# Kernel optimization log

Measured on AMD Instinct MI355X. Metric: run time of the kernel, lower is better.

## Reference

```python
import jax, jax.numpy as jnp
import numpy as np
import math

B, NI, NU, D, H, MAXNB, T = 1024, 50000, 20000, 256, 4, 20, 1000


def _cosine_sqrt_ab():
    t = jnp.linspace(0.0, T, T + 1) / T
    ab = jnp.cos((t + 0.008) / 1.008 * math.pi / 2) ** 2
    ab = ab / ab[0]
    ab = ab[1:]
    return jnp.sqrt(ab), jnp.sqrt(1.0 - ab)


def _ln(x, g, b, eps=1e-5):
    m = jnp.mean(x, -1, keepdims=True)
    v = jnp.var(x, -1, keepdims=True)
    return (x - m) / jnp.sqrt(v + eps) * g + b


def _mha(q, k, v, wqkv, bqkv, wo, bo):
    # torch nn.MultiheadAttention (batch_first) with packed in_proj
    d = q.shape[-1]
    dh = d // H
    wq, wk, wv = jnp.split(wqkv, 3, axis=0)
    bq, bk, bv = jnp.split(bqkv, 3, axis=0)
    def heads(x, w, bb):
        y = x @ w.T + bb
        return y.reshape(x.shape[0], x.shape[1], H, dh).transpose(0, 2, 1, 3)
    qh, kh, vh = heads(q, wq, bq), heads(k, wk, bk), heads(v, wv, bv)
    att = jax.nn.softmax(jnp.einsum('bhqd,bhkd->bhqk', qh, kh) / math.sqrt(dh), axis=-1)
    o = jnp.einsum('bhqk,bhkd->bhqd', att, vh)
    o = o.transpose(0, 2, 1, 3).reshape(q.shape[0], q.shape[1], d)
    return o @ wo.T + bo


def setup_inputs() -> dict:
    key = jax.random.key(0)
    ks = iter(jax.random.split(key, 64))
    p = lambda shape, s=0.02: jax.random.normal(next(ks), shape, jnp.float32) * s
    inp = {}
    inp['x0'] = (jax.random.uniform(next(ks), (B, NI)) < 0.05).astype(jnp.float32)
    inp['user_ids'] = jax.random.randint(next(ks), (B,), 0, NU)
    inp['t'] = jax.random.randint(next(ks), (B,), 0, T)
    inp['noise'] = jax.random.normal(next(ks), (B, D), jnp.float32)
    inp['neighbor_idx'] = jax.random.randint(next(ks), (NU, MAXNB), 0, NI)
    inp['item_emb'] = p((NI, D), 0.01)
    inp['enc_w1'] = p((2 * D, NI), 0.01); inp['enc_b1'] = jnp.zeros((2 * D,))
    inp['enc_w2'] = p((D, 2 * D)); inp['enc_b2'] = jnp.zeros((D,))
    inp['dec_w1'] = p((2 * D, D)); inp['dec_b1'] = jnp.zeros((2 * D,))
    inp['dec_w2'] = p((NI, 2 * D)); inp['dec_b2'] = jnp.zeros((NI,))
    inp['up_w'] = p((D, D)); inp['up_b'] = jnp.zeros((D,))
    inp['ip_w'] = p((D, D)); inp['ip_b'] = jnp.zeros((D,))
    inp['te_w1'] = p((32, 1)); inp['te_b1'] = jnp.zeros((32,))
    inp['te_w2'] = p((D, 32)); inp['te_b2'] = jnp.zeros((D,))
    inp['ca_wqkv'] = p((3 * D, D)); inp['ca_bqkv'] = jnp.zeros((3 * D,))
    inp['ca_wo'] = p((D, D)); inp['ca_bo'] = jnp.zeros((D,))
    inp['sa_wqkv'] = p((3 * D, D)); inp['sa_bqkv'] = jnp.zeros((3 * D,))
    inp['sa_wo'] = p((D, D)); inp['sa_bo'] = jnp.zeros((D,))
    inp['n1_g'] = jnp.ones((D,)); inp['n1_b'] = jnp.zeros((D,))
    inp['n2_g'] = jnp.ones((D,)); inp['n2_b'] = jnp.zeros((D,))
    inp['ff_w1'] = p((2 * D, D)); inp['ff_b1'] = jnp.zeros((2 * D,))
    inp['ff_w2'] = p((D, 2 * D)); inp['ff_b2'] = jnp.zeros((D,))
    return inp


def reference(x0, user_ids, t, noise, neighbor_idx, item_emb,
              enc_w1, enc_b1, enc_w2, enc_b2, dec_w1, dec_b1, dec_w2, dec_b2,
              up_w, up_b, ip_w, ip_b, te_w1, te_b1, te_w2, te_b2,
              ca_wqkv, ca_bqkv, ca_wo, ca_bo, sa_wqkv, sa_bqkv, sa_wo, sa_bo,
              n1_g, n1_b, n2_g, n2_b, ff_w1, ff_b1, ff_w2, ff_b2):
    gelu = lambda x: jax.nn.gelu(x, approximate=False)
    # encoder: (B, NI) -> (B, D)
    z0 = gelu(x0 @ enc_w1.T + enc_b1) @ enc_w2.T + enc_b2
    sqrt_ab, sqrt_1ab = _cosine_sqrt_ab()
    z_t = sqrt_ab[t][:, None] * z0 + sqrt_1ab[t][:, None] * noise
    # vectorized padded neighbor gather: (B, MAXNB, D)
    nb = item_emb[neighbor_idx[user_ids]]
    t_norm = t.astype(jnp.float32) / T
    # denoiser
    q = (z_t @ up_w.T + up_b)[:, None, :]
    kv = nb @ ip_w.T + ip_b
    te = jax.nn.silu(t_norm[:, None] @ te_w1.T + te_b1) @ te_w2.T + te_b2
    q = q + te[:, None, :]
    ca = _mha(q, kv, kv, ca_wqkv, ca_bqkv, ca_wo, ca_bo)
    h = _ln(q + ca, n1_g, n1_b)[:, 0, :]
    sa = _mha(h[:, None], h[:, None], h[:, None], sa_wqkv, sa_bqkv, sa_wo, sa_bo)[:, 0, :]
    h = _ln(h + sa, n2_g, n2_b)
    z_pred = h + (gelu(h @ ff_w1.T + ff_b1) @ ff_w2.T + ff_b2)
    diff_loss = jnp.mean((z_pred - z0) ** 2)
    logits = gelu(z0 @ dec_w1.T + dec_b1) @ dec_w2.T + dec_b2
    recon = jnp.mean(jax.nn.softplus(logits) - logits * x0)
    return diff_loss + 0.1 * recon
```

## Files before the change

### kernel.cpp

```cpp
#include <hip/hip_runtime.h>
#include <math.h>

#define NI   50000
#define Tt   1000
#define KP   50176
#define MW   1568
#define NPAD 50048

typedef __bf16 bf16x8 __attribute__((ext_vector_type(8)));
typedef float  f32x4  __attribute__((ext_vector_type(4)));

__device__ __forceinline__ unsigned short f2bf(float f) {
  unsigned u = __float_as_uint(f);
  u += 0x7FFFu + ((u >> 16) & 1u);
  return (unsigned short)(u >> 16);
}
__device__ __forceinline__ float bf2f(unsigned short u) {
  return __uint_as_float(((unsigned)u) << 16);
}
__device__ __forceinline__ unsigned pack2(float a, float b) {
  return (unsigned)f2bf(a) | ((unsigned)f2bf(b) << 16);
}
__device__ __forceinline__ f32x4 mfma16(const unsigned short* a, const unsigned short* b, f32x4 c) {
  typedef unsigned short u16x8 __attribute__((ext_vector_type(8)));
  u16x8 av = *(const u16x8*)a;
  u16x8 bv = *(const u16x8*)b;
  return __builtin_amdgcn_mfma_f32_16x16x32_bf16(
      __builtin_bit_cast(bf16x8, av), __builtin_bit_cast(bf16x8, bv), c, 0, 0, 0);
}
__device__ __forceinline__ float gelu_f(float x) {
  return 0.5f * x * (1.f + erff(x * 0.70710678118654752f));
}

#define GLD16(gsrc, ldst) __builtin_amdgcn_global_load_lds( \
    (const __attribute__((address_space(1))) unsigned int*)(const void*)(gsrc), \
    (__attribute__((address_space(3))) unsigned int*)(void*)(ldst), 16, 0, 0)
#define GLD4(gsrc, ldst) __builtin_amdgcn_global_load_lds( \
    (const __attribute__((address_space(1))) unsigned int*)(const void*)(gsrc), \
    (__attribute__((address_space(3))) unsigned int*)(void*)(ldst), 4, 0, 0)

#define PIPE_FENCE() __builtin_amdgcn_sched_barrier(0)
#define RAW_BAR()    __builtin_amdgcn_s_barrier()

__global__ __launch_bounds__(256) void prep_crit(
    const float* __restrict__ x0, unsigned int* __restrict__ xmask,
    unsigned int* __restrict__ xmaskT,
    const float* __restrict__ enc_w1, unsigned short* __restrict__ w1b)
{
  __shared__ unsigned int T[32][64];
  __shared__ unsigned int nib[256];
  const int id = blockIdx.x, tid = threadIdx.x;
  if (id < 800) {
    int rg = id / 25, ch = id % 25;
    int r0 = rg * 32, c0 = ch * 2048, c0w = ch * 64;
    for (int rr = 0; rr < 32; ++rr) {
      int k = c0 + tid * 8;
      const float* row = x0 + (size_t)(r0 + rr) * NI;
      float4 a = make_float4(0.f, 0.f, 0.f, 0.f), b = a;
      if (k + 8 <= NI) {
        a = *(const float4*)(row + k);
        b = *(const float4*)(row + k + 4);
      }
      unsigned bits8 =
          (a.x != 0.f ? 1u : 0u)  | (a.y != 0.f ? 2u : 0u)  |
          (a.z != 0.f ? 4u : 0u)  | (a.w != 0.f ? 8u : 0u)  |
          (b.x != 0.f ? 16u : 0u) | (b.y != 0.f ? 32u : 0u) |
          (b.z != 0.f ? 64u : 0u) | (b.w != 0.f ? 128u : 0u);
      nib[tid] = bits8;
      __syncthreads();
      if (tid < 64) {
        T[rr][tid] = nib[tid * 4] | (nib[tid * 4 + 1] << 8) |
                     (nib[tid * 4 + 2] << 16) | (nib[tid * 4 + 3] << 24);
      }
      __syncthreads();
    }
    {
      int rr = tid >> 3, wg = (tid & 7) * 8;
      if (c0w + wg < MW) {
        unsigned* dst = xmask + (size_t)(r0 + rr) * MW + c0w + wg;
        uint4 q0 = make_uint4(T[rr][wg], T[rr][wg+1], T[rr][wg+2], T[rr][wg+3]);
        uint4 q1 = make_uint4(T[rr][wg+4], T[rr][wg+5], T[rr][wg+6], T[rr][wg+7]);
        *(uint4*)dst = q0; *(uint4*)(dst + 4) = q1;
      }
    }
    {
      int ww = tid >> 2, rg8 = (tid & 3) * 8;
      if (c0w + ww < MW) {
        unsigned* dst = xmaskT + (size_t)(c0w + ww) * 1024 + r0 + rg8;
        uint4 q0 = make_uint4(T[rg8][ww], T[rg8+1][ww], T[rg8+2][ww], T[rg8+3][ww]);
        uint4 q1 = make_uint4(T[rg8+4][ww], T[rg8+5][ww], T[rg8+6][ww], T[rg8+7][ww]);
        *(uint4*)dst = q0; *(uint4*)(dst + 4) = q1;
      }
    }
  } else {
    int r = id - 800;
    const float* s = enc_w1 + (size_t)r * NI;
    for (int ch = 0; ch < 25; ++ch) {
      int c = ch * 2048 + tid * 8;
      if (c >= KP) continue;
      uint4 o;
      if (c + 8 <= NI) {
        float4 a = *(const float4*)(s + c), b = *(const float4*)(s + c + 4);
        o.x = pack2(a.x, a.y); o.y = pack2(a.z, a.w);
        o.z = pack2(b.x, b.y); o.w = pack2(b.z, b.w);
      } else {
        float v[8];
#pragma unroll
        for (int i = 0; i < 8; ++i) v[i] = (c + i < NI) ? s[c + i] : 0.f;
        o.x = pack2(v[0], v[1]); o.y = pack2(v[2], v[3]);
        o.z = pack2(v[4], v[5]); o.w = pack2(v[6], v[7]);
      }
      *(uint4*)(w1b + (size_t)r * KP + c) = o;
    }
  }
}

#define EF_ENC  1024
#define EF_W2N  2592
#define EF_MANY 3040
#define EF_COMP 3808
#define EF_TE   4832

__global__ __launch_bounds__(256) void enc_fused(
    const unsigned int* __restrict__ xmaskT,
    const unsigned short* __restrict__ Bw,
    float* __restrict__ P0, float* __restrict__ P1,
    const float* __restrict__ dec_w2, unsigned short* __restrict__ w2n,
    const float* s0a, const float* s1a, const float* s2a, const float* s3a,
    const float* s4a, const float* s5a, const float* s6a,
    unsigned short* d0a, unsigned short* d1a, unsigned short* d2a, unsigned short* d3a,
    unsigned short* d4a, unsigned short* d5a, unsigned short* d6a,
    const float* __restrict__ ca_wqkv, const float* __restrict__ ca_bqkv,
    const float* __restrict__ ip_w, const float* __restrict__ ip_b,
    const float* __restrict__ sa_wqkv, const float* __restrict__ sa_bqkv,
    const float* __restrict__ sa_wo, const float* __restrict__ sa_bo,
    unsigned short* __restrict__ Wkv, float* __restrict__ bkv,
    unsigned short* __restrict__ Wsa, float* __restrict__ bsa,
    const int* __restrict__ t,
    const float* __restrict__ te_w1, const float* __restrict__ te_b1,
    const float* __restrict__ te_w2, const float* __restrict__ te_b2,
    float* __restrict__ te, float* __restrict__ sab, float* __restrict__ s1ab)
{
  __shared__ __align__(16) unsigned short BsE[2][2][128 * 32];
  __shared__ __align__(16) unsigned short lut[256][8];
  __shared__ unsigned int mskb[2][2][128];
  __shared__ float sj[32];
  const int id = blockIdx.x, tid = threadIdx.x;

  if (id < EF_ENC) {
    const int g = (id & 7) + 8 * (id >> 6);
    const int m0 = ((id >> 3) & 7) * 128;
    const int n0 = (g & 3) * 128;
    const int kc = g >> 2;
    const int kb = kc * 1568;
    const int kw0 = kc * 49;
    const int w = tid >> 6, l = tid & 63;
    const int wm = (w >> 1) * 64, wn = (w & 1) * 64;
    const int fr = l & 15, fo = (l >> 4) * 8;
    const int s0 = tid, s1 = tid + 256;
    const unsigned short* Br0 = Bw + (size_t)(n0 + (s0 >> 2)) * KP + kb + (s0 & 3) * 8;
    const unsigned short* Br1 = Bw + (size_t)(n0 + (s1 >> 2)) * KP + kb + (s1 & 3) * 8;
    f32x4 acc[4][4] = {};

    {
      unsigned b = (unsigned)tid;
      uint4 q;
      q.x = (b & 1u   ? 0x3F80u : 0u) | (b & 2u   ? 0x3F800000u : 0u);
      q.y = (b & 4u   ? 0x3F80u : 0u) | (b & 8u   ? 0x3F800000u : 0u);
      q.z = (b & 16u  ? 0x3F80u : 0u) | (b & 32u  ? 0x3F800000u : 0u);
      q.w = (b & 64u  ? 0x3F80u : 0u) | (b & 128u ? 0x3F800000u : 0u);
      *(uint4*)&lut[tid][0] = q;
    }

#define STGF(IT, BUF) do {                                                  \
    GLD4(xmaskT + (size_t)(kw0 + (IT) * 2 + (w & 1)) * 1024                 \
                + m0 + (w >> 1) * 64 + l,                                   \
         &mskb[BUF][w & 1][(w >> 1) * 64]);                                 \
    GLD16(Br0 + (IT) * 64,      &BsE[BUF][0][s0 * 8]);                      \
    GLD16(Br1 + (IT) * 64,      &BsE[BUF][0][s1 * 8]);                      \
    GLD16(Br0 + (IT) * 64 + 32, &BsE[BUF][1][s0 * 8]);                      \
    GLD16(Br1 + (IT) * 64 + 32, &BsE[BUF][1][s1 * 8]); } while (0)

#define STGT(BUF) do {                                                      \
    GLD4(xmaskT + (size_t)(kw0 + 48) * 1024 + m0 + (w & 1) * 64 + l,        \
         &mskb[BUF][0][(w & 1) * 64]);                                      \
    GLD16(Br0 + 24 * 64, &BsE[BUF][0][s0 * 8]);                             \
    GLD16(Br1 + 24 * 64, &BsE[BUF][0][s1 * 8]); } while (0)

#define CMPH(BUF, KK) do {                                                  \
    const unsigned short *ap_[4], *bp_[4];                                  \
    _Pragma("unroll") for (int i_ = 0; i_ < 4; ++i_)                        \
      ap_[i_] = &lut[(mskb[BUF][KK][wm + 16 * i_ + fr] >> fo) & 0xFF][0];   \
    _Pragma("unroll") for (int j_ = 0; j_ < 4; ++j_)                        \
      bp_[j_] = &BsE[BUF][KK][(wn + 16 * j_ + fr) * 32 + fo];               \
    _Pragma("unroll") for (int i_ = 0; i_ < 4; ++i_)                        \
    _Pragma("unroll") for (int j_ = 0; j_ < 4; ++j_)                        \
      acc[i_][j_] = mfma16(ap_[i_], bp_[j_], acc[i_][j_]); } while (0)

    STGF(0, 0);
    STGF(1, 1);
    asm volatile("s_waitcnt vmcnt(5) lgkmcnt(0)" ::: "memory");
    PIPE_FENCE(); RAW_BAR(); PIPE_FENCE();
    for (int it = 0; it < 24; ++it) {
      CMPH(it & 1, 0);
      CMPH(it & 1, 1);
      PIPE_FENCE(); RAW_BAR(); PIPE_FENCE();
      if (it < 22) {
        STGF(it + 2, it & 1);
        asm volatile("s_waitcnt vmcnt(5)" ::: "memory");
      } else if (it == 22) {
        STGT(0);
        asm volatile("s_waitcnt vmcnt(3)" ::: "memory");
      } else {
        asm volatile("s_waitcnt vmcnt(0)" ::: "memory");
      }
      PIPE_FENCE(); RAW_BAR(); PIPE_FENCE();
    }
    CMPH(0, 0);
#undef STGF
#undef STGT
#undef CMPH

    const int cr = (l >> 4) * 4, cc = l & 15;
    float* Cp = ((kc < 16) ? P0 : P1) + (size_t)(kc & 15) * 524288;
#pragma unroll
    for (int i = 0; i < 4; ++i)
#pragma unroll
      for (int j = 0; j < 4; ++j) {
        int n = n0 + wn + 16 * j + cc;
#pragma unroll
        for (int r = 0; r < 4; ++r) {
          int m = m0 + wm + 16 * i + cr + r;
          Cp[(size_t)m * 512 + n] = acc[i][j][r];
        }
      }
  } else if (id < EF_W2N) {
    size_t b2 = id - EF_ENC;
    for (size_t e = (b2 * 256 + tid) * 8; e < 25600000u; e += (size_t)1568 * 256 * 8) {
      float4 a = *(const float4*)(dec_w2 + e), b = *(const float4*)(dec_w2 + e + 4);
      uint4 o;
      o.x = pack2(a.x, a.y); o.y = pack2(a.z, a.w);
      o.z = pack2(b.x, b.y); o.w = pack2(b.z, b.w);
      *(uint4*)(w2n + e) = o;
    }
  } else if (id < EF_MANY) {
    const float* srcs[7] = {s0a, s1a, s2a, s3a, s4a, s5a, s6a};
    unsigned short* dsts[7] = {d0a, d1a, d2a, d3a, d4a, d5a, d6a};
    const int ns[7] = {131072, 65536, 65536, 65536, 131072, 131072, 131072};
    int q = id - EF_W2N;
    int j = q >> 6;
    int i = ((q & 63) * 256 + tid) * 8;
    if (i >= ns[j]) return;
    float4 a = *(const float4*)(srcs[j] + i), b = *(const float4*)(srcs[j] + i + 4);
    uint4 o;
    o.x = pack2(a.x, a.y); o.y = pack2(a.z, a.w);
    o.z = pack2(b.x, b.y); o.w = pack2(b.z, b.w);
    *(uint4*)(dsts[j] + i) = o;
  } else if (id < EF_COMP) {
    int b = id - EF_MANY, k = tid;
    if (b < 512) {
      const float* wrow = ca_wqkv + (size_t)(256 + b) * 256;
      float s = 0.f;
      for (int c = 0; c < 256; ++c) s += wrow[c] * ip_w[c * 256 + k];
      Wkv[b * 256 + k] = f2bf(s);
      if (k == 0) {
        float sb = 0.f;
        for (int c = 0; c < 256; ++c) sb += wrow[c] * ip_b[c];
        bkv[b] = sb + ca_bqkv[256 + b];
      }
    } else {
      int i = b - 512;
      const float* worow = sa_wo + (size_t)i * 256;
      float s = 0.f;
      for (int c = 0; c < 256; ++c) s += worow[c] * sa_wqkv[(512 + c) * 256 + k];
      Wsa[i * 256 + k] = f2bf(s);
      if (k == 0) {
        float sb = 0.f;
        for (int c = 0; c < 256; ++c) sb += worow[c] * sa_bqkv[512 + c];
        bsa[i] = sb + sa_bo[i];
      }
    }
  } else {
    int b = id - EF_COMP, d = tid;
    int ti = t[b];
    float tn = (float)ti / (float)Tt;
    if (d < 32) {
      float a = tn * te_w1[d] + te_b1[d];
      sj[d] = a / (1.f + __expf(-a));
    }
    if (d == 0) {
      double tt = (double)(ti + 1) / (double)Tt;
      double c  = cos((tt + 0.008) / 1.008 * M_PI * 0.5);
      double c0 = cos((0.008) / 1.008 * M_PI * 0.5);
      double ab = (c * c) / (c0 * c0);
      sab[b]  = (float)sqrt(ab);
      s1ab[b] = (float)sqrt(1.0 - ab);
    }
    __syncthreads();
    float accv = te_b2[d];
#pragma unroll
    for (int j = 0; j < 32; ++j) accv += sj[j] * te_w2[d * 32 + j];
    te[(size_t)b * 256 + d] = accv;
  }
}

template<int T>
__global__ __launch_bounds__(256) void gemm128(
    const unsigned short* __restrict__ A, int lda,
    const unsigned short* __restrict__ Bw, int ldb,
    const float* __restrict__ bias, void* __restrict__ Cv, int ldc, int K,
    const unsigned int* __restrict__ xmask, float* __restrict__ loss, int Nvalid)
{
  __shared__ __align__(16) unsigned short As[128 * 32];
  __shared__ __align__(16) unsigned short Bs[128 * 32];
  __shared__ unsigned int msk[128][4];
  __shared__ float red[4];
  const int tid = threadIdx.x;
  int m0, n0, iters;
  if (T == 1) {
    int id = blockIdx.x;
    int n = (id & 7) + 8 * (id >> 6);
    if (n >= 391) return;
    m0 = ((id >> 3) & 7) * 128;
    n0 = n * 128;
    iters = 16;
  } else {
    m0 = blockIdx.x * 128; n0 = blockIdx.y * 128;
    iters = K >> 5;
  }
  const int w = tid >> 6, l = tid & 63;
  const int wm = (w >> 1) * 64, wn = (w & 1) * 64;
  const int fr = l & 15, fo = (l >> 4) * 8;
  const int s0 = tid, s1 = tid + 256;
  f32x4 acc[4][4] = {};
  for (int it = 0; it < iters; ++it) {
    int k0 = it * 32;
    __syncthreads();
    GLD16(A  + (size_t)(m0 + (s0 >> 2)) * lda + k0 + (s0 & 3) * 8, &As[s0 * 8]);
    GLD16(A  + (size_t)(m0 + (s1 >> 2)) * lda + k0 + (s1 & 3) * 8, &As[s1 * 8]);
    GLD16(Bw + (size_t)(n0 + (s0 >> 2)) * ldb + k0 + (s0 & 3) * 8, &Bs[s0 * 8]);
    GLD16(Bw + (size_t)(n0 + (s1 >> 2)) * ldb + k0 + (s1 & 3) * 8, &Bs[s1 * 8]);
    __syncthreads();
    const unsigned short *ap[4], *bp[4];
#pragma unroll
    for (int i = 0; i < 4; ++i) {
      ap[i] = &As[(wm + 16 * i + fr) * 32 + fo];
      bp[i] = &Bs[(wn + 16 * i + fr) * 32 + fo];
    }
#pragma unroll
    for (int i = 0; i < 4; ++i)
#pragma unroll
      for (int j = 0; j < 4; ++j)
        acc[i][j] = mfma16(ap[i], bp[j], acc[i][j]);
  }
  const int cr = (l >> 4) * 4, cc = l & 15;
  if (T == 0) {
    unsigned short* Cb = (unsigned short*)Cv;
#pragma unroll
    for (int j = 0; j < 4; ++j) {
      int n = n0 + wn + 16 * j + cc;
      float bv = bias[n];
#pragma unroll
      for (int i = 0; i < 4; ++i)
#pragma unroll
        for (int r = 0; r < 4; ++r) {
          int m = m0 + wm + 16 * i + cr + r;
          Cb[(size_t)m * ldc + n] = f2bf(acc[i][j][r] + bv);
        }
    }
  } else {
    {
      int row = tid >> 1, p = tid & 1;
      *(uint2*)&msk[row][p * 2] =
          *(const uint2*)(xmask + (size_t)(m0 + row) * MW + (n0 >> 5) + p * 2);
    }
    __syncthreads();
    float ts = 0.f;
#pragma unroll
    for (int j = 0; j < 4; ++j) {
      int nl = wn + 16 * j + cc;
      int n = n0 + nl;
      if (n < Nvalid) {
        float bv = bias[n];
#pragma unroll
        for (int i = 0; i < 4; ++i)
#pragma unroll
          for (int r = 0; r < 4; ++r) {
            int ml = wm + 16 * i + cr + r;
            float lg = acc[i][j][r] + bv;
            float sp = fmaxf(lg, 0.f) + __logf(1.f + __expf(-fabsf(lg)));
            unsigned word = msk[ml][nl >> 5];
            ts += sp - (((word >> (nl & 31)) & 1u) ? lg : 0.f);
          }
      }
    }
    for (int off = 32; off > 0; off >>= 1) ts += __shfl_xor(ts, off);
    if (l == 0) red[w] = ts;
    __syncthreads();
    if (tid == 0) atomicAdd(loss, red[0] + red[1] + red[2] + red[3]);
  }
}

template<int EPI>
__global__ __launch_bounds__(256) void gemm64(
    const unsigned short* __restrict__ A, int lda,
    const unsigned short* __restrict__ Bw, int ldb,
    const float* __restrict__ bias, void* __restrict__ Cv, int ldc, int K,
    const void* __restrict__ R0, const void* __restrict__ R1, const void* __restrict__ R2,
    void* __restrict__ W0, void* __restrict__ W1, float* __restrict__ loss)
{
  __shared__ __align__(16) unsigned short As[64 * 32];
  __shared__ __align__(16) unsigned short Bs[64 * 32];
  __shared__ float red[4];
  const int tid = threadIdx.x;
  const int m0 = blockIdx.x * 64, n0 = blockIdx.y * 64;
  const int w = tid >> 6, l = tid & 63;
  const int wm = (w >> 1) * 32, wn = (w & 1) * 32;
  const int fr = l & 15, fo = (l >> 4) * 8;
  const int srow = tid >> 2, scol = (tid & 3) * 8;
  f32x4 acc[2][2] = {};
  for (int k0 = 0; k0 < K; k0 += 32) {
    __syncthreads();
    GLD16(A  + (size_t)(m0 + srow) * lda + k0 + scol, &As[tid * 8]);
    GLD16(Bw + (size_t)(n0 + srow) * ldb + k0 + scol, &Bs[tid * 8]);
    __syncthreads();
    const unsigned short* ap0 = &As[(wm +      fr) * 32 + fo];
    const unsigned short* ap1 = &As[(wm + 16 + fr) * 32 + fo];
    const unsigned short* bp0 = &Bs[(wn +      fr) * 32 + fo];
    const unsigned short* bp1 = &Bs[(wn + 16 + fr) * 32 + fo];
    acc[0][0] = mfma16(ap0, bp0, acc[0][0]);
    acc[0][1] = mfma16(ap0, bp1, acc[0][1]);
    acc[1][0] = mfma16(ap1, bp0, acc[1][0]);
    acc[1][1] = mfma16(ap1, bp1, acc[1][1]);
  }
  const int cr = (l >> 4) * 4, cc = l & 15;
  float ts = 0.f;
#pragma unroll
  for (int i = 0; i < 2; ++i)
#pragma unroll
    for (int j = 0; j < 2; ++j) {
      int n = n0 + wn + 16 * j + cc;
      float bv = bias[n];
#pragma unroll
      for (int r = 0; r < 4; ++r) {
        int m = m0 + wm + 16 * i + cr + r;
        float v = acc[i][j][r] + bv;
        size_t idx = (size_t)m * ldc + n;
        if (EPI == 0) ((float*)Cv)[idx] = v;
        if (EPI == 1) ((unsigned short*)Cv)[idx] = f2bf(v);
        if (EPI == 2) ((unsigned short*)Cv)[idx] = f2bf(gelu_f(v));
        if (EPI == 3) {
          ((float*)Cv)[idx] = v;
          ((unsigned short*)W0)[idx] = f2bf(v);
          float zt = ((const float*)R1)[m] * v +
                     ((const float*)R2)[m] * ((const float*)R0)[idx];
          ((unsigned short*)W1)[idx] = f2bf(zt);
        }
        if (EPI == 4) {
          v += ((const float*)R0)[idx];
          ((unsigned short*)Cv)[idx] = f2bf(v);
        }
        if (EPI == 5) {
          v += bf2f(((const unsigned short*)R0)[idx]);
          float d = v - ((const float*)R1)[idx];
          ts += d * d;
        }
      }
    }
  if (EPI == 5) {
    for (int off = 32; off > 0; off >>= 1) ts += __shfl_xor(ts, off);
    if (l == 0) red[w] = ts;
    __syncthreads();
    if (tid == 0) atomicAdd(loss, red[0] + red[1] + red[2] + red[3]);
  }
}

__global__ __launch_bounds__(256) void h1_epi(const float* __restrict__ P0,
                                              const float* __restrict__ P1,
                                              const float* __restrict__ b,
                                              unsigned short* __restrict__ H) {
  int i = blockIdx.x * 256 + threadIdx.x;
  float s = b[i & 511];
#pragma unroll
  for (int k = 0; k < 16; ++k) s += P0[(size_t)k * 524288 + i];
#pragma unroll
  for (int k = 0; k < 16; ++k) s += P1[(size_t)k * 524288 + i];
  H[i] = f2bf(gelu_f(s));
}

__global__ __launch_bounds__(256) void gather_nb(
    const int* __restrict__ uid, const int* __restrict__ nidx,
    const float* __restrict__ emb, unsigned short* __restrict__ nb)
{
  int b = blockIdx.x, d = threadIdx.x;
  const int* np = nidx + uid[b] * 20;
#pragma unroll
  for (int j = 0; j < 20; ++j) {
    int idx = np[j];
    nb[((size_t)b * 20 + j) * 256 + d] = f2bf(emb[(size_t)idx * 256 + d]);
  }
}

__global__ __launch_bounds__(256) void attn_k(
    const float* __restrict__ qh, const unsigned short* __restrict__ kvh,
    unsigned short* __restrict__ o)
{
  int b = blockIdx.x, tid = threadIdx.x;
  int h = tid >> 6, d = tid & 63;
  float qv = qh[(size_t)b * 256 + h * 64 + d];
  const unsigned short* kbase = kvh + (size_t)b * 20 * 512 + h * 64 + d;
  const unsigned short* vbase = kbase + 256;
  float s[20];
#pragma unroll
  for (int k = 0; k < 20; ++k) {
    float p = qv * bf2f(kbase[k * 512]);
    for (int off = 32; off > 0; off >>= 1) p += __shfl_xor(p, off);
    s[k] = p * 0.125f;
  }
  float mx = s[0];
#pragma unroll
  for (int k = 1; k < 20; ++k) mx = fmaxf(mx, s[k]);
  float sum = 0.f;
#pragma unroll
  for (int k = 0; k < 20; ++k) { s[k] = __expf(s[k] - mx); sum += s[k]; }
  float inv = 1.f / sum;
  float ov = 0.f;
#pragma unroll
  for (int k = 0; k < 20; ++k) ov += s[k] * bf2f(vbase[k * 512]);
  o[(size_t)b * 256 + h * 64 + d] = f2bf(ov * inv);
}

__global__ __launch_bounds__(256) void ln_k(
    const unsigned short* __restrict__ X, const unsigned short* __restrict__ Y,
    const float* __restrict__ g, const float* __restrict__ bb,
    unsigned short* __restrict__ out)
{
  __shared__ float rs[4], rs2[4];
  int b = blockIdx.x, d = threadIdx.x;
  size_t i = (size_t)b * 256 + d;
  float v = bf2f(X[i]) + bf2f(Y[i]);
  float s = v, s2 = v * v;
  for (int off = 32; off > 0; off >>= 1) { s += __shfl_xor(s, off); s2 += __shfl_xor(s2, off); }
  int w = d >> 6, l = d & 63;
  if (l == 0) { rs[w] = s; rs2[w] = s2; }
  __syncthreads();
  s  = rs[0] + rs[1] + rs[2] + rs[3];
  s2 = rs2[0] + rs2[1] + rs2[2] + rs2[3];
  float mean = s * (1.f / 256.f);
  float var  = s2 * (1.f / 256.f) - mean * mean;
  out[i] = f2bf((v - mean) * rsqrtf(var + 1e-5f) * g[d] + bb[d]);
}

__global__ void final_k(const float* __restrict__ scal, float* __restrict__ out) {
  out[0] = scal[0] * (1.f / (1024.f * 256.f)) + 0.1f * scal[1] * (1.f / (1024.f * 50000.f));
}

extern "C" void kernel_launch(void* const* d_in, const int* in_sizes, int n_in,
                              void* d_out, int out_size, void* d_ws, size_t ws_size,
                              hipStream_t stream) {
  const float* x0      = (const float*)d_in[0];
  const int*   uid     = (const int*)  d_in[1];
  const int*   t       = (const int*)  d_in[2];
  const float* noise   = (const float*)d_in[3];
  const int*   nidx    = (const int*)  d_in[4];
  const float* item_emb= (const float*)d_in[5];
  const float* enc_w1  = (const float*)d_in[6];
  const float* enc_b1  = (const float*)d_in[7];
  const float* enc_w2  = (const float*)d_in[8];
  const float* enc_b2  = (const float*)d_in[9];
  const float* dec_w1  = (const float*)d_in[10];
  const float* dec_b1  = (const float*)d_in[11];
  const float* dec_w2  = (const float*)d_in[12];
  const float* dec_b2  = (const float*)d_in[13];
  const float* up_w    = (const float*)d_in[14];
  const float* up_b    = (const float*)d_in[15];
  const float* ip_w    = (const float*)d_in[16];
  const float* ip_b    = (const float*)d_in[17];
  const float* te_w1   = (const float*)d_in[18];
  const float* te_b1   = (const float*)d_in[19];
  const float* te_w2   = (const float*)d_in[20];
  const float* te_b2   = (const float*)d_in[21];
  const float* ca_wqkv = (const float*)d_in[22];
  const float* ca_bqkv = (const float*)d_in[23];
  const float* ca_wo   = (const float*)d_in[24];
  const float* ca_bo   = (const float*)d_in[25];
  const float* sa_wqkv = (const float*)d_in[26];
  const float* sa_bqkv = (const float*)d_in[27];
  const float* sa_wo   = (const float*)d_in[28];
  const float* sa_bo   = (const float*)d_in[29];
  const float* n1_g    = (const float*)d_in[30];
  const float* n1_b    = (const float*)d_in[31];
  const float* n2_g    = (const float*)d_in[32];
  const float* n2_b    = (const float*)d_in[33];
  const float* ff_w1   = (const float*)d_in[34];
  const float* ff_b1   = (const float*)d_in[35];
  const float* ff_w2   = (const float*)d_in[36];
  const float* ff_b2   = (const float*)d_in[37];
  (void)in_sizes; (void)n_in; (void)out_size; (void)ws_size;

  float* ws   = (float*)d_ws;
  float* scal = ws;
  float* sab  = ws + 4;
  float* s1ab = sab + 1024;
  float* te   = s1ab + 1024;
  float* qhf  = te + 262144;
  float* z0f  = qhf + 262144;
  float* bkv  = z0f + 262144;
  float* bsa  = bkv + 512;
  unsigned int* xmask = (unsigned int*)(bsa + 256);
  unsigned short* sh  = (unsigned short*)(xmask + 1024 * MW);
  float*          OUTp = (float*)sh;
  unsigned short* nbb  = sh;
  unsigned short* kvhb = nbb + 5242880;
  unsigned short* f1b  = kvhb + 10485760;
  unsigned short* Gb   = f1b + 524288;
  unsigned short* x0b  = Gb + 524288;
  unsigned short* w2n  = x0b;
  unsigned int*   xmaskT = (unsigned int*)(x0b + 26214400);
  unsigned short* w1b  = x0b + (size_t)1024 * KP;
  unsigned short* H1b  = w1b + (size_t)512 * KP;
  unsigned short* z0b  = H1b + 524288;
  unsigned short* ztb  = z0b + 262144;
  unsigned short* qpb  = ztb + 262144;
  unsigned short* ob   = qpb + 262144;
  unsigned short* cab  = ob  + 262144;
  unsigned short* hb   = cab + 262144;
  unsigned short* saob = hb  + 262144;
  unsigned short* h2b  = saob+ 262144;
  unsigned short* enc_w2b = h2b + 262144;
  unsigned short* up_wb   = enc_w2b + 131072;
  unsigned short* ca_wqb  = up_wb + 65536;
  unsigned short* ca_wob  = ca_wqb + 65536;
  unsigned short* ff_w1b  = ca_wob + 65536;
  unsigned short* ff_w2b  = ff_w1b + 131072;
  unsigned short* dec_w1b = ff_w2b + 131072;
  unsigned short* Wkv     = dec_w1b + 131072;
  unsigned short* Wsab    = Wkv + 131072;
  float*          OUTp2   = (float*)(Wsab + 131072);

  hipMemsetAsync(scal, 0, 4 * sizeof(float), stream);

  prep_crit<<<1312, 256, 0, stream>>>(x0, xmask, xmaskT, enc_w1, w1b);

  enc_fused<<<EF_TE, 256, 0, stream>>>(
      xmaskT, w1b, OUTp, OUTp2,
      dec_w2, w2n,
      enc_w2, up_w, ca_wqkv, ca_wo, ff_w1, ff_w2, dec_w1,
      enc_w2b, up_wb, ca_wqb, ca_wob, ff_w1b, ff_w2b, dec_w1b,
      ca_wqkv, ca_bqkv, ip_w, ip_b, sa_wqkv, sa_bqkv, sa_wo, sa_bo,
      Wkv, bkv, Wsab, bsa,
      t, te_w1, te_b1, te_w2, te_b2, te, sab, s1ab);
  h1_epi<<<2048, 256, 0, stream>>>(OUTp, OUTp2, enc_b1, H1b);

  gather_nb<<<1024, 256, 0, stream>>>(uid, nidx, item_emb, nbb);
  gemm128<0><<<dim3(160, 4), 256, 0, stream>>>(
      nbb, 256, Wkv, 256, bkv, kvhb, 512, 256, nullptr, nullptr, 0);

  gemm64<3><<<dim3(16, 4), 256, 0, stream>>>(
      H1b, 512, enc_w2b, 512, enc_b2, z0f, 256, 512, noise, sab, s1ab, z0b, ztb, nullptr);

  gemm64<4><<<dim3(16, 4), 256, 0, stream>>>(
      ztb, 256, up_wb, 256, up_b, qpb, 256, 256, te, nullptr, nullptr, nullptr, nullptr, nullptr);
  gemm64<0><<<dim3(16, 4), 256, 0, stream>>>(
      qpb, 256, ca_wqb, 256, ca_bqkv, qhf, 256, 256,
      nullptr, nullptr, nullptr, nullptr, nullptr, nullptr);

  attn_k<<<1024, 256, 0, stream>>>(qhf, kvhb, ob);
  gemm64<1><<<dim3(16, 4), 256, 0, stream>>>(
      ob, 256, ca_wob, 256, ca_bo, cab, 256, 256,
      nullptr, nullptr, nullptr, nullptr, nullptr, nullptr);
  ln_k<<<1024, 256, 0, stream>>>(qpb, cab, n1_g, n1_b, hb);

  gemm64<1><<<dim3(16, 4), 256, 0, stream>>>(
      hb, 256, Wsab, 256, bsa, saob, 256, 256,
      nullptr, nullptr, nullptr, nullptr, nullptr, nullptr);
  ln_k<<<1024, 256, 0, stream>>>(hb, saob, n2_g, n2_b, h2b);

  gemm64<2><<<dim3(16, 8), 256, 0, stream>>>(
      h2b, 256, ff_w1b, 256, ff_b1, f1b, 512, 256,
      nullptr, nullptr, nullptr, nullptr, nullptr, nullptr);
  gemm64<5><<<dim3(16, 4), 256, 0, stream>>>(
      f1b, 512, ff_w2b, 512, ff_b2, nullptr, 256, 512,
      h2b, z0f, nullptr, nullptr, nullptr, &scal[0]);

  gemm64<2><<<dim3(16, 8), 256, 0, stream>>>(
      z0b, 256, dec_w1b, 256, dec_b1, Gb, 512, 256,
      nullptr, nullptr, nullptr, nullptr, nullptr, nullptr);
  gemm128<1><<<3136, 256, 0, stream>>>(
      Gb, 512, w2n, 512, dec_b2, nullptr, 0, 512, xmask, &scal[1], NI);

  final_k<<<1, 1, 0, stream>>>(scal, (float*)d_out);
}
```

Baseline: 827.7 us.

## Split prep_crit into finer-grained blocks for bitmask packing and weight conversion

Reworks the prep kernel so each thread builds a full 32-bit mask word directly from 32 consecutive floats, removing the per-row loop with two barriers per row. The mask tiles become 32 rows by 8 words, using one barrier before the transposed write. The enc_w1 bf16 conversion is also split from one block per row into 25 blocks per row, raising the grid from 1312 to 19072 blocks. The aim is more memory-level parallelism on a bandwidth-bound prep pass, at the cost of less coalesced loads (each thread reads 128 contiguous bytes) and small 4-byte stores.

```diff
diff --git a/kernel.cpp b/kernel.cpp
--- a/kernel.cpp
+++ b/kernel.cpp
@@ -42,76 +42,62 @@
 #define PIPE_FENCE() __builtin_amdgcn_sched_barrier(0)
 #define RAW_BAR()    __builtin_amdgcn_s_barrier()
 
+#define PC_BM 6272
+#define PC_W1 19072
+
 __global__ __launch_bounds__(256) void prep_crit(
     const float* __restrict__ x0, unsigned int* __restrict__ xmask,
     unsigned int* __restrict__ xmaskT,
     const float* __restrict__ enc_w1, unsigned short* __restrict__ w1b)
 {
-  __shared__ unsigned int T[32][64];
-  __shared__ unsigned int nib[256];
+  __shared__ unsigned int T[32][8];
   const int id = blockIdx.x, tid = threadIdx.x;
-  if (id < 800) {
-    int rg = id / 25, ch = id % 25;
-    int r0 = rg * 32, c0 = ch * 2048, c0w = ch * 64;
-    for (int rr = 0; rr < 32; ++rr) {
-      int k = c0 + tid * 8;
-      const float* row = x0 + (size_t)(r0 + rr) * NI;
-      float4 a = make_float4(0.f, 0.f, 0.f, 0.f), b = a;
-      if (k + 8 <= NI) {
-        a = *(const float4*)(row + k);
-        b = *(const float4*)(row + k + 4);
+  if (id < PC_BM) {
+    const int rg = id / 196, wc = id % 196;
+    const int r0 = rg * 32, w0 = wc * 8;
+    const int rr = tid >> 3, wd = tid & 7;
+    const int row = r0 + rr;
+    const int gw = w0 + wd;
+    const int cb = gw * 32;
+    const float* rp = x0 + (size_t)row * NI + cb;
+    unsigned wv = 0;
+    if (cb + 32 <= NI) {
+#pragma unroll
+      for (int k = 0; k < 8; ++k) {
+        float4 v = *(const float4*)(rp + k * 4);
+        wv |= (v.x != 0.f ? 1u : 0u) << (k * 4) |
+              (v.y != 0.f ? 2u : 0u) << (k * 4) |
+              (v.z != 0.f ? 4u : 0u) << (k * 4) |
+              (v.w != 0.f ? 8u : 0u) << (k * 4);
       }
-      unsigned bits8 =
-          (a.x != 0.f ? 1u : 0u)  | (a.y != 0.f ? 2u : 0u)  |
-          (a.z != 0.f ? 4u : 0u)  | (a.w != 0.f ? 8u : 0u)  |
-          (b.x != 0.f ? 16u : 0u) | (b.y != 0.f ? 32u : 0u) |
-          (b.z != 0.f ? 64u : 0u) | (b.w != 0.f ? 128u : 0u);
-      nib[tid] = bits8;
-      __syncthreads();
-      if (tid < 64) {
-        T[rr][tid] = nib[tid * 4] | (nib[tid * 4 + 1] << 8) |
-                     (nib[tid * 4 + 2] << 16) | (nib[tid * 4 + 3] << 24);
-      }
-      __syncthreads();
-    }
-    {
-      int rr = tid >> 3, wg = (tid & 7) * 8;
-      if (c0w + wg < MW) {
-        unsigned* dst = xmask + (size_t)(r0 + rr) * MW + c0w + wg;
-        uint4 q0 = make_uint4(T[rr][wg], T[rr][wg+1], T[rr][wg+2], T[rr][wg+3]);
-        uint4 q1 = make_uint4(T[rr][wg+4], T[rr][wg+5], T[rr][wg+6], T[rr][wg+7]);
-        *(uint4*)dst = q0; *(uint4*)(dst + 4) = q1;
-      }
-    }
-    {
-      int ww = tid >> 2, rg8 = (tid & 3) * 8;
-      if (c0w + ww < MW) {
-        unsigned* dst = xmaskT + (size_t)(c0w + ww) * 1024 + r0 + rg8;
-        uint4 q0 = make_uint4(T[rg8][ww], T[rg8+1][ww], T[rg8+2][ww], T[rg8+3][ww]);
-        uint4 q1 = make_uint4(T[rg8+4][ww], T[rg8+5][ww], T[rg8+6][ww], T[rg8+7][ww]);
-        *(uint4*)dst = q0; *(uint4*)(dst + 4) = q1;
-      }
-    }
+    } else {
+      for (int k = 0; k < 32; ++k)
+        if (cb + k < NI && rp[k] != 0.f) wv |= 1u << k;
+    }
+    T[rr][wd] = wv;
+    xmask[(size_t)row * MW + gw] = wv;
+    __syncthreads();
+    int wq = tid >> 5, r2 = tid & 31;
+    xmaskT[(size_t)(w0 + wq) * 1024 + r0 + r2] = T[r2][wq];
   } else {
-    int r = id - 800;
+    int q = id - PC_BM;
+    int r = q / 25, ch = q % 25;
+    int c = ch * 2048 + tid * 8;
+    if (c >= KP) return;
     const float* s = enc_w1 + (size_t)r * NI;
-    for (int ch = 0; ch < 25; ++ch) {
-      int c = ch * 2048 + tid * 8;
-      if (c >= KP) continue;
-      uint4 o;
-      if (c + 8 <= NI) {
-        float4 a = *(const float4*)(s + c), b = *(const float4*)(s + c + 4);
-        o.x = pack2(a.x, a.y); o.y = pack2(a.z, a.w);
-        o.z = pack2(b.x, b.y); o.w = pack2(b.z, b.w);
-      } else {
-        float v[8];
-#pragma unroll
-        for (int i = 0; i < 8; ++i) v[i] = (c + i < NI) ? s[c + i] : 0.f;
-        o.x = pack2(v[0], v[1]); o.y = pack2(v[2], v[3]);
-        o.z = pack2(v[4], v[5]); o.w = pack2(v[6], v[7]);
-      }
-      *(uint4*)(w1b + (size_t)r * KP + c) = o;
-    }
+    uint4 o;
+    if (c + 8 <= NI) {
+      float4 a = *(const float4*)(s + c), b = *(const float4*)(s + c + 4);
+      o.x = pack2(a.x, a.y); o.y = pack2(a.z, a.w);
+      o.z = pack2(b.x, b.y); o.w = pack2(b.z, b.w);
+    } else {
+      float v[8];
+#pragma unroll
+      for (int i = 0; i < 8; ++i) v[i] = (c + i < NI) ? s[c + i] : 0.f;
+      o.x = pack2(v[0], v[1]); o.y = pack2(v[2], v[3]);
+      o.z = pack2(v[4], v[5]); o.w = pack2(v[6], v[7]);
+    }
+    *(uint4*)(w1b + (size_t)r * KP + c) = o;
   }
 }
 
@@ -640,7 +626,7 @@
 
   hipMemsetAsync(scal, 0, 4 * sizeof(float), stream);
 
-  prep_crit<<<1312, 256, 0, stream>>>(x0, xmask, xmaskT, enc_w1, w1b);
+  prep_crit<<<PC_W1, 256, 0, stream>>>(x0, xmask, xmaskT, enc_w1, w1b);
 
   enc_fused<<<EF_TE, 256, 0, stream>>>(
       xmaskT, w1b, OUTp, OUTp2,
```

Measured after the change: 810.6 us. -2.1%, faster.
